# Performance work log

Measured on AMD Instinct MI355X. Metric: run time of the kernel, lower is better.

The kernel has to match this reference:

```python
import jax, jax.numpy as jnp
import numpy as np

NV, NE = 4096, 8192
FV, FE = 128, 64
FV_OUT = 128


def setup_inputs() -> dict:
    key = jax.random.key(0)
    ks = jax.random.split(key, 8)
    stdv = 1.0 / np.sqrt(FV_OUT)
    return {
        "H_v": jax.random.normal(ks[0], (NV, FV), dtype=jnp.float32),
        "H_e": jax.random.normal(ks[1], (NE, FE), dtype=jnp.float32),
        "adj_e": jax.random.uniform(ks[2], (NE, NE), dtype=jnp.float32),
        "adj_v": jax.random.uniform(ks[3], (NV, NV), dtype=jnp.float32),
        "T": jax.random.uniform(ks[4], (NV, NE), dtype=jnp.float32),
        "weight": jax.random.uniform(ks[5], (FV, FV_OUT), minval=-stdv, maxval=stdv, dtype=jnp.float32),
        "p": jax.random.normal(ks[6], (1, FE), dtype=jnp.float32),
        "bias": jax.random.uniform(ks[7], (FV_OUT,), minval=-stdv, maxval=stdv, dtype=jnp.float32),
    }


def reference(H_v, H_e, adj_e, adj_v, T, weight, p, bias):
    # node_layer=True path of GraphConvolution.forward
    # d = (H_e @ p.T) as a vector over edges; T @ diag(d) == T * d[None, :]
    d = (H_e @ p.T)[:, 0]                       # [Ne]
    multiplier = (T * d[None, :]) @ T.T         # [Nv, Nv]
    n = multiplier.shape[0]
    mask = jnp.eye(n, dtype=multiplier.dtype)   # eye mask: diag -> 1, off-diag -> multiplier
    M1 = mask + (1.0 - mask) * multiplier
    adjusted_A = M1 * adj_v                     # elementwise mask with dense adjacency
    output = adjusted_A @ (H_v @ weight) + bias # [Nv, Fv_out]
    return (output, H_e)
```

## Files before the change

### kernel.cpp

```cpp
#include <hip/hip_runtime.h>
#include <stdint.h>

#define NV 4096
#define NE 8192
#define FV 128
#define FE 64
#define FOUT 128

typedef unsigned short u16;
typedef __attribute__((ext_vector_type(8))) short short8;
typedef __attribute__((ext_vector_type(4))) float f32x4;
typedef __attribute__((ext_vector_type(4))) unsigned short u16x4;

__device__ __forceinline__ u16 f2bf(float f) {
  uint32_t u = __builtin_bit_cast(uint32_t, f);
  u += 0x7fffu + ((u >> 16) & 1u);
  return (u16)(u >> 16);
}
__device__ __forceinline__ float bf2f(u16 h) {
  return __builtin_bit_cast(float, (uint32_t)h << 16);
}

#define AS1(p) ((__attribute__((address_space(1))) void*)(void*)(p))
#define AS3(p) ((__attribute__((address_space(3))) void*)(p))

__global__ __launch_bounds__(64) void k_edge_dot(const float* __restrict__ He,
                                                 const float* __restrict__ p,
                                                 float* __restrict__ d) {
  int e = blockIdx.x;
  int l = threadIdx.x;
  float v = He[e * FE + l] * p[l];
  #pragma unroll
  for (int off = 32; off > 0; off >>= 1) v += __shfl_down(v, off);
  if (l == 0) d[e] = v;
}

__global__ __launch_bounds__(256) void k_convert(const float* __restrict__ T,
                                                 const float* __restrict__ d,
                                                 u16* __restrict__ Ta,
                                                 u16* __restrict__ Tb) {
  size_t idx = ((size_t)blockIdx.x * 256 + threadIdx.x) * 4;
  f32x4 t = *(const f32x4*)&T[idx];
  int e = (int)(idx & (NE - 1));
  f32x4 dv = *(const f32x4*)&d[e];
  u16x4 a, b;
  a.x = f2bf(t.x * dv.x); a.y = f2bf(t.y * dv.y);
  a.z = f2bf(t.z * dv.z); a.w = f2bf(t.w * dv.w);
  b.x = f2bf(t.x); b.y = f2bf(t.y); b.z = f2bf(t.z); b.w = f2bf(t.w);
  *(u16x4*)&Ta[idx] = a;
  *(u16x4*)&Tb[idx] = b;
}

__global__ __launch_bounds__(128) void k_hw(const float* __restrict__ Hv,
                                            const float* __restrict__ W,
                                            u16* __restrict__ HWt) {
  __shared__ float sh[FV];
  int i = blockIdx.x;
  int n = threadIdx.x;
  sh[n] = Hv[i * FV + n];
  __syncthreads();
  float s = 0.f;
  #pragma unroll
  for (int f = 0; f < FV; ++f) s += sh[f] * W[f * FOUT + n];
  HWt[(size_t)n * NV + i] = f2bf(s);
}

__global__ __launch_bounds__(256) void k_init_out(float* __restrict__ out,
                                                  const float* __restrict__ bias,
                                                  const float* __restrict__ He) {
  int idx = blockIdx.x * 256 + threadIdx.x;
  if (idx < NV * FOUT) out[idx] = bias[idx & (FOUT - 1)];
  else out[idx] = He[idx - NV * FOUT];
}

__global__ __launch_bounds__(256) void k_gemm_mult(const u16* __restrict__ Ta,
                                                   const u16* __restrict__ Tb,
                                                   const float* __restrict__ adjv,
                                                   u16* __restrict__ adjA) {
  __shared__ __align__(16) u16 smem[128 * 136];
  u16* lA = smem;
  u16* lB = smem + 4096;
  u16* sT = smem;

  int id = blockIdx.x;
  int bi = (int)((sqrtf(8.0f * (float)id + 1.0f) - 1.0f) * 0.5f);
  while ((bi + 1) * (bi + 2) / 2 <= id) ++bi;
  while (bi * (bi + 1) / 2 > id) --bi;
  int bj = id - bi * (bi + 1) / 2;

  const int K = NE;
  const int tile_m = bi * 128;
  const int tile_n = bj * 128;
  const int tid = threadIdx.x;
  const int lane = tid & 63;
  const int wave = tid >> 6;
  const int wm = (wave >> 1) * 64;
  const int wn = (wave & 1) * 64;
  const int row16 = lane & 15;
  const int quad = lane >> 4;

  f32x4 acc[4][4] = {};

  for (int k0 = 0; k0 < K; k0 += 32) {
    __syncthreads();
    #pragma unroll
    for (int r = 0; r < 2; ++r) {
      const int chunk = r * 256 + wave * 64 + lane;
      const int row = chunk >> 2;
      const int cc = chunk & 3;
      const u16* ga = Ta + ((size_t)(tile_m + row) * K + k0 + cc * 8);
      const u16* gb = Tb + ((size_t)(tile_n + row) * K + k0 + cc * 8);
      __builtin_amdgcn_global_load_lds(AS1(ga), AS3(&lA[(r * 256 + wave * 64) * 8]), 16, 0, 0);
      __builtin_amdgcn_global_load_lds(AS1(gb), AS3(&lB[(r * 256 + wave * 64) * 8]), 16, 0, 0);
    }
    __syncthreads();
    short8 a[4], b[4];
    #pragma unroll
    for (int mi = 0; mi < 4; ++mi)
      a[mi] = *(const short8*)&lA[(wm + mi * 16 + row16) * 32 + quad * 8];
    #pragma unroll
    for (int ni = 0; ni < 4; ++ni)
      b[ni] = *(const short8*)&lB[(wn + ni * 16 + row16) * 32 + quad * 8];
    #pragma unroll
    for (int mi = 0; mi < 4; ++mi)
      #pragma unroll
      for (int ni = 0; ni < 4; ++ni)
        acc[mi][ni] = __builtin_amdgcn_mfma_f32_16x16x32_bf16(a[mi], b[ni], acc[mi][ni], 0, 0, 0);
  }

  #pragma unroll
  for (int mi = 0; mi < 4; ++mi) {
    #pragma unroll
    for (int ni = 0; ni < 4; ++ni) {
      const int gc = tile_n + wn + ni * 16 + row16;
      #pragma unroll
      for (int r = 0; r < 4; ++r) {
        const int gr = tile_m + wm + mi * 16 + quad * 4 + r;
        float v = acc[mi][ni][r];
        if (gr == gc) v = 1.0f;
        v *= adjv[(size_t)gr * NV + gc];
        adjA[(size_t)gr * NV + gc] = f2bf(v);
      }
    }
  }

  if (bi != bj) {
    __syncthreads();
    #pragma unroll
    for (int mi = 0; mi < 4; ++mi) {
      #pragma unroll
      for (int ni = 0; ni < 4; ++ni) {
        const int c = wn + ni * 16 + row16;
        const int r0 = wm + mi * 16 + quad * 4;
        u16x4 pk;
        pk.x = f2bf(acc[mi][ni][0]); pk.y = f2bf(acc[mi][ni][1]);
        pk.z = f2bf(acc[mi][ni][2]); pk.w = f2bf(acc[mi][ni][3]);
        *(u16x4*)&sT[c * 136 + r0] = pk;
      }
    }
    __syncthreads();
    const int row = tid >> 1;
    const int half = tid & 1;
    const size_t obase = (size_t)(tile_n + row) * NV + tile_m + half * 64;
    const u16* srow = &sT[row * 136 + half * 64];
    #pragma unroll
    for (int j = 0; j < 8; ++j) {
      short8 m8 = *(const short8*)&srow[j * 8];
      short8 o8;
      #pragma unroll
      for (int k = 0; k < 8; ++k) {
        float v = bf2f((u16)m8[k]) * adjv[obase + j * 8 + k];
        o8[k] = (short)f2bf(v);
      }
      *(short8*)&adjA[obase + j * 8] = o8;
    }
  }
}

#define KSPLIT 16
__global__ __launch_bounds__(256) void k_gemm_out(const u16* __restrict__ A,
                                                  const u16* __restrict__ B,
                                                  float* __restrict__ out) {
  __shared__ __align__(16) u16 lA[128 * 32];
  __shared__ __align__(16) u16 lB[128 * 32];
  const int K = NV;
  const int tile_m = blockIdx.y * 128;
  const int kbeg = blockIdx.x * (K / KSPLIT);
  const int kend = kbeg + (K / KSPLIT);
  const int tid = threadIdx.x;
  const int lane = tid & 63;
  const int wave = tid >> 6;
  const int wm = (wave >> 1) * 64;
  const int wn = (wave & 1) * 64;
  const int row16 = lane & 15;
  const int quad = lane >> 4;

  f32x4 acc[4][4] = {};

  for (int k0 = kbeg; k0 < kend; k0 += 32) {
    __syncthreads();
    #pragma unroll
    for (int r = 0; r < 2; ++r) {
      const int chunk = r * 256 + wave * 64 + lane;
      const int row = chunk >> 2;
      const int cc = chunk & 3;
      const u16* ga = A + ((size_t)(tile_m + row) * K + k0 + cc * 8);
      const u16* gb = B + ((size_t)row * K + k0 + cc * 8);
      __builtin_amdgcn_global_load_lds(AS1(ga), AS3(&lA[(r * 256 + wave * 64) * 8]), 16, 0, 0);
      __builtin_amdgcn_global_load_lds(AS1(gb), AS3(&lB[(r * 256 + wave * 64) * 8]), 16, 0, 0);
    }
    __syncthreads();
    short8 a[4], b[4];
    #pragma unroll
    for (int mi = 0; mi < 4; ++mi)
      a[mi] = *(const short8*)&lA[(wm + mi * 16 + row16) * 32 + quad * 8];
    #pragma unroll
    for (int ni = 0; ni < 4; ++ni)
      b[ni] = *(const short8*)&lB[(wn + ni * 16 + row16) * 32 + quad * 8];
    #pragma unroll
    for (int mi = 0; mi < 4; ++mi)
      #pragma unroll
      for (int ni = 0; ni < 4; ++ni)
        acc[mi][ni] = __builtin_amdgcn_mfma_f32_16x16x32_bf16(a[mi], b[ni], acc[mi][ni], 0, 0, 0);
  }

  #pragma unroll
  for (int mi = 0; mi < 4; ++mi) {
    #pragma unroll
    for (int ni = 0; ni < 4; ++ni) {
      const int gc = wn + ni * 16 + row16;
      #pragma unroll
      for (int r = 0; r < 4; ++r) {
        const int gr = tile_m + wm + mi * 16 + quad * 4 + r;
        atomicAdd(&out[(size_t)gr * FOUT + gc], acc[mi][ni][r]);
      }
    }
  }
}

extern "C" void kernel_launch(void* const* d_in, const int* in_sizes, int n_in,
                              void* d_out, int out_size, void* d_ws, size_t ws_size,
                              hipStream_t stream) {
  const float* Hv   = (const float*)d_in[0];
  const float* He   = (const float*)d_in[1];
  const float* adjv = (const float*)d_in[3];
  const float* T    = (const float*)d_in[4];
  const float* W    = (const float*)d_in[5];
  const float* p    = (const float*)d_in[6];
  const float* bias = (const float*)d_in[7];
  float* out = (float*)d_out;

  char* ws = (char*)d_ws;
  float* dvec = (float*)ws;
  u16* HWt  = (u16*)(ws + ((size_t)1 << 20));
  u16* Ta   = (u16*)(ws + ((size_t)2 << 20));
  u16* Tb   = (u16*)(ws + ((size_t)2 << 20) + ((size_t)64 << 20));
  u16* adjA = (u16*)(ws + ((size_t)2 << 20) + ((size_t)128 << 20));

  k_edge_dot<<<NE, 64, 0, stream>>>(He, p, dvec);
  k_convert<<<(NV * NE) / (256 * 4), 256, 0, stream>>>(T, dvec, Ta, Tb);
  k_hw<<<NV, 128, 0, stream>>>(Hv, W, HWt);
  k_init_out<<<(NV * FOUT + NE * FE) / 256, 256, 0, stream>>>(out, bias, He);
  k_gemm_mult<<<(32 * 33) / 2, 256, 0, stream>>>(Ta, Tb, adjv, adjA);
  k_gemm_out<<<dim3(KSPLIT, NV / 128), 256, 0, stream>>>(adjA, HWt, out);
}
```

Before: 827.7 us.

## Split-K the symmetric multiplier GEMM and move masking into a separate kernel

The triangular T·diag(d)·Tᵀ GEMM now runs as 1056 blocks, each pair of blocks splitting K in half, instead of 528 blocks, to fill more compute units. Each half writes its partial tile as bf16 to a workspace buffer. A new mask kernel sums the two partials, applies the diagonal and adjacency masks, and writes both the tile and its transpose. This adds an extra launch and partial-result traffic, and it rounds the partials to bf16 before they are summed.

New measurement: 733.1 us. -11.4%, faster.

```diff
diff --git a/kernel.cpp b/kernel.cpp
--- a/kernel.cpp
+++ b/kernel.cpp
@@ -23,6 +23,13 @@
 
 #define AS1(p) ((__attribute__((address_space(1))) void*)(void*)(p))
 #define AS3(p) ((__attribute__((address_space(3))) void*)(p))
+
+__device__ __forceinline__ void tri_decode(int id, int& bi, int& bj) {
+  bi = (int)((sqrtf(8.0f * (float)id + 1.0f) - 1.0f) * 0.5f);
+  while ((bi + 1) * (bi + 2) / 2 <= id) ++bi;
+  while (bi * (bi + 1) / 2 > id) --bi;
+  bj = id - bi * (bi + 1) / 2;
+}
 
 __global__ __launch_bounds__(64) void k_edge_dot(const float* __restrict__ He,
                                                  const float* __restrict__ p,
@@ -73,22 +80,20 @@
   else out[idx] = He[idx - NV * FOUT];
 }
 
-__global__ __launch_bounds__(256) void k_gemm_mult(const u16* __restrict__ Ta,
-                                                   const u16* __restrict__ Tb,
-                                                   const float* __restrict__ adjv,
-                                                   u16* __restrict__ adjA) {
-  __shared__ __align__(16) u16 smem[128 * 136];
-  u16* lA = smem;
-  u16* lB = smem + 4096;
-  u16* sT = smem;
-
-  int id = blockIdx.x;
-  int bi = (int)((sqrtf(8.0f * (float)id + 1.0f) - 1.0f) * 0.5f);
-  while ((bi + 1) * (bi + 2) / 2 <= id) ++bi;
-  while (bi * (bi + 1) / 2 > id) --bi;
-  int bj = id - bi * (bi + 1) / 2;
+__global__ __launch_bounds__(256) void k_gemm_sym(const u16* __restrict__ Ta,
+                                                  const u16* __restrict__ Tb,
+                                                  u16* __restrict__ Mp) {
+  __shared__ __align__(16) u16 lA[128 * 32];
+  __shared__ __align__(16) u16 lB[128 * 32];
+  const int bx = blockIdx.x;
+  const int pair = bx >> 1;
+  const int split = bx & 1;
+  int bi, bj;
+  tri_decode(pair, bi, bj);
 
   const int K = NE;
+  const int kbeg = split * (K / 2);
+  const int kend = kbeg + K / 2;
   const int tile_m = bi * 128;
   const int tile_n = bj * 128;
   const int tid = threadIdx.x;
@@ -101,7 +106,7 @@
 
   f32x4 acc[4][4] = {};
 
-  for (int k0 = 0; k0 < K; k0 += 32) {
+  for (int k0 = kbeg; k0 < kend; k0 += 32) {
     __syncthreads();
     #pragma unroll
     for (int r = 0; r < 2; ++r) {
@@ -128,6 +133,55 @@
         acc[mi][ni] = __builtin_amdgcn_mfma_f32_16x16x32_bf16(a[mi], b[ni], acc[mi][ni], 0, 0, 0);
   }
 
+  u16* dst = Mp + (size_t)bx * 16384 + wave * 4096;
+  #pragma unroll
+  for (int mi = 0; mi < 4; ++mi) {
+    #pragma unroll
+    for (int ni = 0; ni < 4; ++ni) {
+      const int f = mi * 4 + ni;
+      u16x4 pk;
+      pk.x = f2bf(acc[mi][ni][0]); pk.y = f2bf(acc[mi][ni][1]);
+      pk.z = f2bf(acc[mi][ni][2]); pk.w = f2bf(acc[mi][ni][3]);
+      *(u16x4*)&dst[f * 256 + lane * 4] = pk;
+    }
+  }
+}
+
+__global__ __launch_bounds__(256) void k_mask(const u16* __restrict__ Mp,
+                                              const float* __restrict__ adjv,
+                                              u16* __restrict__ adjA) {
+  __shared__ __align__(16) u16 sT[128 * 136];
+  const int pair = blockIdx.x;
+  int bi, bj;
+  tri_decode(pair, bi, bj);
+  const int tile_m = bi * 128;
+  const int tile_n = bj * 128;
+  const int tid = threadIdx.x;
+  const int lane = tid & 63;
+  const int wave = tid >> 6;
+  const int wm = (wave >> 1) * 64;
+  const int wn = (wave & 1) * 64;
+  const int row16 = lane & 15;
+  const int quad = lane >> 4;
+
+  const u16* s0 = Mp + (size_t)(pair * 2) * 16384 + wave * 4096;
+  const u16* s1 = s0 + 16384;
+
+  f32x4 acc[4][4];
+  #pragma unroll
+  for (int mi = 0; mi < 4; ++mi) {
+    #pragma unroll
+    for (int ni = 0; ni < 4; ++ni) {
+      const int f = mi * 4 + ni;
+      u16x4 a = *(const u16x4*)&s0[f * 256 + lane * 4];
+      u16x4 b = *(const u16x4*)&s1[f * 256 + lane * 4];
+      acc[mi][ni][0] = bf2f(a.x) + bf2f(b.x);
+      acc[mi][ni][1] = bf2f(a.y) + bf2f(b.y);
+      acc[mi][ni][2] = bf2f(a.z) + bf2f(b.z);
+      acc[mi][ni][3] = bf2f(a.w) + bf2f(b.w);
+    }
+  }
+
   #pragma unroll
   for (int mi = 0; mi < 4; ++mi) {
     #pragma unroll
@@ -145,7 +199,6 @@
   }
 
   if (bi != bj) {
-    __syncthreads();
     #pragma unroll
     for (int mi = 0; mi < 4; ++mi) {
       #pragma unroll
@@ -256,11 +309,13 @@
   u16* Ta   = (u16*)(ws + ((size_t)2 << 20));
   u16* Tb   = (u16*)(ws + ((size_t)2 << 20) + ((size_t)64 << 20));
   u16* adjA = (u16*)(ws + ((size_t)2 << 20) + ((size_t)128 << 20));
+  u16* Mp   = (u16*)(ws + ((size_t)2 << 20) + ((size_t)160 << 20));
 
   k_edge_dot<<<NE, 64, 0, stream>>>(He, p, dvec);
   k_convert<<<(NV * NE) / (256 * 4), 256, 0, stream>>>(T, dvec, Ta, Tb);
   k_hw<<<NV, 128, 0, stream>>>(Hv, W, HWt);
   k_init_out<<<(NV * FOUT + NE * FE) / 256, 256, 0, stream>>>(out, bias, He);
-  k_gemm_mult<<<(32 * 33) / 2, 256, 0, stream>>>(Ta, Tb, adjv, adjA);
+  k_gemm_sym<<<528 * 2, 256, 0, stream>>>(Ta, Tb, Mp);
+  k_mask<<<528, 256, 0, stream>>>(Mp, adjv, adjA);
   k_gemm_out<<<dim3(KSPLIT, NV / 128), 256, 0, stream>>>(adjA, HWt, out);
 }
```
